# Kernel optimization log

Measured on AMD Instinct MI355X. Metric: run time of the kernel, lower is better.

Reference implementation:

```python
import jax, jax.numpy as jnp
import numpy as np

B, S, HID, NH = 2, 2048, 1024, 16
HD = HID // NH
SCALE = HD ** -0.5


def elu_plus_one(x):
    return jax.nn.elu(x) + 1.0


def setup_inputs() -> dict:
    key = jax.random.key(0)
    ks = jax.random.split(key, 8)
    w_scale = 0.02  # keep logits in a sane range
    return {
        "hidden_states": jax.random.normal(ks[0], (B, S, HID), jnp.float32),
        "wq": jax.random.normal(ks[1], (HID, HID), jnp.float32) * w_scale,
        "wk": jax.random.normal(ks[2], (HID, HID), jnp.float32) * w_scale,
        "wv": jax.random.normal(ks[3], (HID, HID), jnp.float32) * w_scale,
        "wo": jax.random.normal(ks[4], (HID, HID), jnp.float32) * w_scale,
        "beta": jax.random.normal(ks[5], (NH,), jnp.float32),
        "memory": jax.random.normal(ks[6], (NH, HD, HD), jnp.float32),
        "memory_norm": jax.random.uniform(ks[7], (NH, HD), jnp.float32),
    }


def reference(hidden_states, wq, wk, wv, wo, beta, memory, memory_norm):
    b, s, _ = hidden_states.shape
    # nn.Linear(bias=False): x @ W^T; weights stored [out, in]
    def proj(x, w):
        return jnp.einsum("bsh,oh->bso", x, w).reshape(b, s, NH, HD).transpose(0, 2, 1, 3)

    q = proj(hidden_states, wq)  # [B,H,S,D]
    k = proj(hidden_states, wk)
    v = proj(hidden_states, wv)

    # local causal softmax attention (materializes [B,H,S,S] as the original does)
    scores = jnp.einsum("bhsd,bhtd->bhst", q, k) * SCALE
    causal_mask = jnp.triu(jnp.full((s, s), -jnp.inf, dtype=scores.dtype), k=1)
    attn = jax.nn.softmax(scores + causal_mask, axis=-1)
    a_local = jnp.einsum("bhst,bhtd->bhsd", attn, v)

    # compressive memory retrieval: sigma(Q) @ M / (sigma(Q) @ z)
    sigma_q = elu_plus_one(q)
    a_mem_unnorm = jnp.einsum("bhsd,hde->bhse", sigma_q, memory)
    norm = jnp.clip(jnp.einsum("bhsd,hd->bhs", sigma_q, memory_norm), 1e-6, None)
    a_mem = a_mem_unnorm / norm[..., None]

    gate = jax.nn.sigmoid(beta).reshape(1, NH, 1, 1)
    combined = gate * a_mem + (1.0 - gate) * a_local  # [B,H,S,D]
    combined = combined.transpose(0, 2, 1, 3).reshape(b, s, HID)
    return jnp.einsum("bsh,oh->bso", combined, wo)
```

## Files before the change

kernel.cpp:

```cpp
#include <hip/hip_runtime.h>
#include <stdint.h>

#define LOG2E 1.4426950408889634f

typedef __attribute__((ext_vector_type(8))) __bf16 bf16x8;
typedef __attribute__((ext_vector_type(4))) __bf16 bf16x4;
typedef __attribute__((ext_vector_type(4))) float f32x4;

__device__ inline void gll16(const void* g, void* l) {
  __builtin_amdgcn_global_load_lds(
      (const __attribute__((address_space(1))) void*)g,
      (__attribute__((address_space(3))) void*)l, 16, 0, 0);
}

__global__ __launch_bounds__(256) void cvt_all(
    const float* __restrict__ hs, const float* __restrict__ wq,
    const float* __restrict__ wk, const float* __restrict__ wv,
    const float* __restrict__ wo,
    __bf16* __restrict__ hsb, __bf16* __restrict__ wqb, __bf16* __restrict__ wkb,
    __bf16* __restrict__ wvb, __bf16* __restrict__ wob) {
  int bid = blockIdx.x;
  const float* s; __bf16* d; int i;
  if (bid < 4096) { s = hs; d = hsb; i = bid * 256 + threadIdx.x; }
  else {
    int seg = (bid - 4096) >> 10;
    i = ((bid - 4096) & 1023) * 256 + threadIdx.x;
    s = seg == 0 ? wq : seg == 1 ? wk : seg == 2 ? wv : wo;
    d = seg == 0 ? wqb : seg == 1 ? wkb : seg == 2 ? wvb : wob;
  }
  float4 v = ((const float4*)s)[i];
  bf16x4 o;
  o[0] = (__bf16)v.x; o[1] = (__bf16)v.y; o[2] = (__bf16)v.z; o[3] = (__bf16)v.w;
  *(bf16x4*)&d[(size_t)i * 4] = o;
}

#define KSCALE 0.18033688011112042f
__global__ __launch_bounds__(256, 3) void qkv_gemm(
    const __bf16* __restrict__ hsb, const __bf16* __restrict__ wqb,
    const __bf16* __restrict__ wkb, const __bf16* __restrict__ wvb,
    __bf16* __restrict__ qbuf, __bf16* __restrict__ kbuf,
    __bf16* __restrict__ vtb) {
  constexpr int K = 1024;
  __shared__ __align__(16) __bf16 lta[128 * 32];
  __shared__ __align__(16) __bf16 ltb[128 * 32];
  const int bid = blockIdx.x;
  const int z = bid >> 8, r = bid & 255;
  const __bf16 *A, *Bt;
  int m0, n0;
  if (z < 2) {
    A = hsb; Bt = z ? wkb : wqb;
    m0 = (r & 31) * 128; n0 = (r >> 5) * 128;
  } else {
    A = wvb; Bt = hsb;
    m0 = (r & 7) * 128; n0 = (r >> 3) * 128;
  }
  const int tid = threadIdx.x;
  const int w = tid >> 6, l = tid & 63;
  const int lg = l >> 4, lr = l & 15;
  const int wm = (w >> 1) * 64, wn = (w & 1) * 64;
  f32x4 acc[4][4] = {};
  const int srow = w * 16 + (l >> 2);
  const int scol = (l & 3) * 8;
  const __bf16* ga = A + (size_t)(m0 + srow) * K + scol;
  const __bf16* gb = Bt + (size_t)(n0 + srow) * K + scol;
  __bf16* la = &lta[(size_t)w * 16 * 32];
  __bf16* lb = &ltb[(size_t)w * 16 * 32];
  for (int k0 = 0; k0 < K; k0 += 32) {
    __syncthreads();
    gll16(ga + k0, la);
    gll16(ga + 64 * K + k0, la + 64 * 32);
    gll16(gb + k0, lb);
    gll16(gb + 64 * K + k0, lb + 64 * 32);
    __syncthreads();
    bf16x8 af[4], bfr[4];
#pragma unroll
    for (int i = 0; i < 4; ++i) {
      af[i]  = *(const bf16x8*)&lta[(wm + i * 16 + lr) * 32 + lg * 8];
      bfr[i] = *(const bf16x8*)&ltb[(wn + i * 16 + lr) * 32 + lg * 8];
    }
#pragma unroll
    for (int i = 0; i < 4; ++i)
#pragma unroll
      for (int j = 0; j < 4; ++j)
        acc[i][j] = __builtin_amdgcn_mfma_f32_16x16x32_bf16(af[i], bfr[j], acc[i][j], 0, 0, 0);
  }
#pragma unroll
  for (int i = 0; i < 4; ++i)
#pragma unroll
    for (int j = 0; j < 4; ++j)
#pragma unroll
      for (int rr = 0; rr < 4; ++rr) {
        int gm = m0 + wm + i * 16 + lg * 4 + rr;
        int gn = n0 + wn + j * 16 + lr;
        float v = acc[i][j][rr];
        if (z < 2) {
          int bb = gm >> 11, s = gm & 2047, hh = gn >> 6, d = gn & 63;
          __bf16* dst = z ? kbuf : qbuf;
          if (z) v *= KSCALE;
          dst[(((size_t)bb * 16 + hh) * 2048 + s) * 64 + d] = (__bf16)v;
        } else {
          int bb = gn >> 11, s = gn & 2047, hh = gm >> 6, d = gm & 63;
          vtb[(((size_t)bb * 16 + hh) * 64 + d) * 2048 + s] = (__bf16)v;
        }
      }
}

__global__ __launch_bounds__(256, 2) void gemm_out(const __bf16* __restrict__ A,
                                                   const __bf16* __restrict__ Bt,
                                                   float* __restrict__ C,
                                                   int M, int N) {
  constexpr int K = 1024;
  __shared__ __align__(16) __bf16 lta[128 * 32];
  __shared__ __align__(16) __bf16 ltb[64 * 32];
  const int tid = threadIdx.x;
  const int w = tid >> 6, l = tid & 63;
  const int lg = l >> 4, lr = l & 15;
  const int m0 = blockIdx.x * 128, n0 = blockIdx.y * 64;
  const int wm = (w >> 1) * 64, wn = (w & 1) * 32;
  f32x4 acc[4][2] = {};
  const int srow = tid >> 2;
  const int scol = (tid & 3) * 8;
  const __bf16* ga = A + (size_t)(m0 + srow) * K + scol;
  const __bf16* gb = Bt + (size_t)(n0 + srow) * K + scol;
  __bf16* la = &lta[(size_t)w * 512];
  __bf16* lb = &ltb[(size_t)w * 512];
  for (int k0 = 0; k0 < K; k0 += 32) {
    __syncthreads();
    gll16(ga + k0, la);
    gll16(ga + (size_t)64 * K + k0, la + 64 * 32);
    gll16(gb + k0, lb);
    __syncthreads();
    bf16x8 af[4], bfr[2];
#pragma unroll
    for (int i = 0; i < 4; ++i)
      af[i]  = *(const bf16x8*)&lta[(wm + i * 16 + lr) * 32 + lg * 8];
#pragma unroll
    for (int j = 0; j < 2; ++j)
      bfr[j] = *(const bf16x8*)&ltb[(wn + j * 16 + lr) * 32 + lg * 8];
#pragma unroll
    for (int i = 0; i < 4; ++i)
#pragma unroll
      for (int j = 0; j < 2; ++j)
        acc[i][j] = __builtin_amdgcn_mfma_f32_16x16x32_bf16(af[i], bfr[j], acc[i][j], 0, 0, 0);
  }
#pragma unroll
  for (int i = 0; i < 4; ++i)
#pragma unroll
    for (int j = 0; j < 2; ++j)
#pragma unroll
      for (int rr = 0; rr < 4; ++rr) {
        int gm = m0 + wm + i * 16 + lg * 4 + rr;
        int gn = n0 + wn + j * 16 + lr;
        C[(size_t)gm * N + gn] = acc[i][j][rr];
      }
}

#define DEFER_THR 11.5f
#define SWZ(row, col) (((row) << 7) + ((col) ^ (((row) & 7) << 3)))
#define SWZK(row, col) (((row) << 6) + ((col) ^ (((row) & 7) << 3)))

__global__ __launch_bounds__(256, 2) void attn_kernel(
    const __bf16* __restrict__ qb,
    const __bf16* __restrict__ kb,
    const __bf16* __restrict__ vtb,
    const float* __restrict__ memory,
    const float* __restrict__ memnorm,
    const float* __restrict__ beta,
    __bf16* __restrict__ comb)
{
  __shared__ __align__(16) __bf16 kt[128 * 64];
  __shared__ __align__(16) __bf16 vt[64 * 128];
  __shared__ __align__(16) __bf16 pt[4][16 * 128];

  const int tid = threadIdx.x;
  const int w = tid >> 6, l = tid & 63;
  const int lg = l >> 4, lr = l & 15;
  const int tt = blockIdx.x >> 5;
  const int t = (tt < 8) ? (15 - tt) : (tt - 8);
  const int bh = blockIdx.x & 31;
  const int hh = bh & 15, b = bh >> 4;
  const int wq0 = t * 128 + w * 32;
  const int ntiles = t + 1;

  const int k_row = tid >> 3;
  const int k_col = ((tid & 7) ^ (k_row & 7)) * 8;
  const __bf16* ksrc = kb + ((size_t)bh * 2048 + k_row) * 64 + k_col;
  const int v_d = tid >> 4;
  const int v_col = ((tid & 15) ^ (v_d & 7)) * 8;
  const __bf16* vsrc = vtb + ((size_t)bh * 64 + v_d) * 2048 + v_col;
  __bf16* kdst = &kt[w * 512];
  __bf16* vdst = &vt[w * 512];

  bf16x8 qf[2][2];
#pragma unroll
  for (int mf = 0; mf < 2; ++mf)
#pragma unroll
    for (int kk = 0; kk < 2; ++kk)
      qf[mf][kk] = *(const bf16x8*)(qb + ((size_t)bh * 2048 + wq0 + mf * 16 + lr) * 64 + kk * 32 + lg * 8);

  float mrun[2] = {-1e30f, -1e30f}, lsum[2] = {0.f, 0.f};
  f32x4 apv[2][4] = {};

  for (int kv = 0; kv < ntiles; ++kv) {
    const int kv0 = kv * 128;
    __syncthreads();
#pragma unroll
    for (int i = 0; i < 4; ++i) {
      gll16(ksrc + (size_t)(kv0 + i * 32) * 64, kdst + i * 2048);
      gll16(vsrc + (size_t)i * 16 * 2048 + kv0, vdst + i * 2048);
    }
    __syncthreads();

    f32x4 sc[2][8] = {};
#pragma unroll
    for (int kk = 0; kk < 2; ++kk)
#pragma unroll
      for (int nf = 0; nf < 8; ++nf) {
        bf16x8 kf = *(const bf16x8*)&kt[SWZK(nf * 16 + lr, kk * 32 + lg * 8)];
#pragma unroll
        for (int mf = 0; mf < 2; ++mf)
          sc[mf][nf] = __builtin_amdgcn_mfma_f32_16x16x32_bf16(kf, qf[mf][kk], sc[mf][nf], 0, 0, 0);
      }

    if (kv == ntiles - 1) {
#pragma unroll
      for (int mf = 0; mf < 2; ++mf) {
        const int qrow = wq0 + mf * 16 + lr;
#pragma unroll
        for (int nf = 0; nf < 8; ++nf)
#pragma unroll
          for (int r = 0; r < 4; ++r)
            if (kv0 + nf * 16 + lg * 4 + r > qrow) sc[mf][nf][r] = -1e30f;
      }
    }

#pragma unroll
    for (int mf = 0; mf < 2; ++mf) {
      f32x4 m4 = sc[mf][0];
#pragma unroll
      for (int nf = 1; nf < 8; ++nf)
#pragma unroll
        for (int r = 0; r < 4; ++r) m4[r] = fmaxf(m4[r], sc[mf][nf][r]);
      float mx = fmaxf(fmaxf(m4[0], m4[1]), fmaxf(m4[2], m4[3]));
      mx = fmaxf(mx, __shfl_xor(mx, 16, 64));
      mx = fmaxf(mx, __shfl_xor(mx, 32, 64));
      if (!__all(mx - mrun[mf] <= DEFER_THR)) {
        float mold = mrun[mf];
        float mn = fmaxf(mold, mx);
        mrun[mf] = mn;
        float scl = __builtin_amdgcn_exp2f(mold - mn);
        lsum[mf] *= scl;
        float sclq[4];
#pragma unroll
        for (int r = 0; r < 4; ++r) sclq[r] = __shfl(scl, (lg << 2) | r, 16);
#pragma unroll
        for (int nf = 0; nf < 4; ++nf)
#pragma unroll
          for (int r = 0; r < 4; ++r) apv[mf][nf][r] *= sclq[r];
      }
    }

    bf16x8 pa0[4];
    {
      float rs = 0.f;
#pragma unroll
      for (int nf = 0; nf < 8; ++nf) {
        bf16x4 pk;
#pragma unroll
        for (int r = 0; r < 4; ++r) {
          float pv = __builtin_amdgcn_exp2f(sc[0][nf][r] - mrun[0]);
          rs += pv;
          pk[r] = (__bf16)pv;
        }
        *(bf16x4*)&pt[w][SWZ(lr, nf * 16 + lg * 4)] = pk;
      }
      rs += __shfl_xor(rs, 16, 64);
      rs += __shfl_xor(rs, 32, 64);
      lsum[0] += rs;
#pragma unroll
      for (int kk = 0; kk < 4; ++kk)
        pa0[kk] = *(const bf16x8*)&pt[w][SWZ(lr, kk * 32 + lg * 8)];
    }
    {
      float rs = 0.f;
#pragma unroll
      for (int nf = 0; nf < 8; ++nf) {
        bf16x4 pk;
#pragma unroll
        for (int r = 0; r < 4; ++r) {
          float pv = __builtin_amdgcn_exp2f(sc[1][nf][r] - mrun[1]);
          rs += pv;
          pk[r] = (__bf16)pv;
        }
        *(bf16x4*)&pt[w][SWZ(lr, nf * 16 + lg * 4)] = pk;
      }
      rs += __shfl_xor(rs, 16, 64);
      rs += __shfl_xor(rs, 32, 64);
      lsum[1] += rs;
    }

#pragma unroll
    for (int kk = 0; kk < 4; ++kk) {
      bf16x8 pa1 = *(const bf16x8*)&pt[w][SWZ(lr, kk * 32 + lg * 8)];
#pragma unroll
      for (int nf = 0; nf < 4; ++nf) {
        bf16x8 vf = *(const bf16x8*)&vt[SWZ(nf * 16 + lr, kk * 32 + lg * 8)];
        apv[0][nf] = __builtin_amdgcn_mfma_f32_16x16x32_bf16(pa0[kk], vf, apv[0][nf], 0, 0, 0);
        apv[1][nf] = __builtin_amdgcn_mfma_f32_16x16x32_bf16(pa1, vf, apv[1][nf], 0, 0, 0);
      }
    }
  }

  __syncthreads();
  __bf16* mt = kt;
  for (int i = tid; i < 64 * 64; i += 256) {
    int d = i >> 6, e = i & 63;
    mt[e * 72 + d] = (__bf16)memory[((size_t)hh * 64 + d) * 64 + e];
  }
  for (int i = tid; i < 16 * 64; i += 256) {
    int e = 64 + (i >> 6), d = i & 63;
    mt[e * 72 + d] = (__bf16)memnorm[hh * 64 + d];
  }
  __syncthreads();

  bf16x8 sf[2][2];
#pragma unroll
  for (int mf = 0; mf < 2; ++mf)
#pragma unroll
    for (int kk = 0; kk < 2; ++kk) {
      bf16x8 q = qf[mf][kk], s;
#pragma unroll
      for (int j = 0; j < 8; ++j) {
        float x = (float)q[j];
        float sg = x > 0.f ? x + 1.f : __builtin_amdgcn_exp2f(x * LOG2E);
        s[j] = (__bf16)sg;
      }
      sf[mf][kk] = s;
    }

  f32x4 am[2][5] = {};
#pragma unroll
  for (int kk = 0; kk < 2; ++kk)
#pragma unroll
    for (int nf = 0; nf < 5; ++nf) {
      bf16x8 bb = *(const bf16x8*)&mt[(nf * 16 + lr) * 72 + kk * 32 + lg * 8];
#pragma unroll
      for (int mf = 0; mf < 2; ++mf)
        am[mf][nf] = __builtin_amdgcn_mfma_f32_16x16x32_bf16(sf[mf][kk], bb, am[mf][nf], 0, 0, 0);
    }

  const float gate = 1.f / (1.f + __builtin_amdgcn_exp2f(-beta[hh] * LOG2E));
  const float og = 1.f - gate;
#pragma unroll
  for (int mf = 0; mf < 2; ++mf) {
    float lsq[4];
#pragma unroll
    for (int r = 0; r < 4; ++r) lsq[r] = __shfl(lsum[mf], (lg << 2) | r, 16);
#pragma unroll
    for (int r = 0; r < 4; ++r) {
      int row = wq0 + mf * 16 + lg * 4 + r;
      float linv = __builtin_amdgcn_rcpf(lsq[r]);
      float nrm = fmaxf(am[mf][4][r], 1e-6f);
      float ninv = __builtin_amdgcn_rcpf(nrm);
      size_t base = ((size_t)b * 2048 + row) * 1024 + hh * 64;
#pragma unroll
      for (int nf = 0; nf < 4; ++nf)
        comb[base + nf * 16 + lr] =
            (__bf16)(gate * am[mf][nf][r] * ninv + og * apv[mf][nf][r] * linv);
    }
  }
}

extern "C" void kernel_launch(void* const* d_in, const int* in_sizes, int n_in,
                              void* d_out, int out_size, void* d_ws, size_t ws_size,
                              hipStream_t stream) {
  const float* hs      = (const float*)d_in[0];
  const float* wq      = (const float*)d_in[1];
  const float* wk      = (const float*)d_in[2];
  const float* wv      = (const float*)d_in[3];
  const float* wo      = (const float*)d_in[4];
  const float* beta    = (const float*)d_in[5];
  const float* memory  = (const float*)d_in[6];
  const float* memnorm = (const float*)d_in[7];
  float* out = (float*)d_out;

  char* ws = (char*)d_ws;
  __bf16* hsb  = (__bf16*)(ws);
  __bf16* wqb  = (__bf16*)(ws + ((size_t)8  << 20));
  __bf16* wkb  = (__bf16*)(ws + ((size_t)10 << 20));
  __bf16* wvb  = (__bf16*)(ws + ((size_t)12 << 20));
  __bf16* wob  = (__bf16*)(ws + ((size_t)14 << 20));
  __bf16* qbuf = (__bf16*)(ws + ((size_t)16 << 20));
  __bf16* kbuf = (__bf16*)(ws + ((size_t)24 << 20));
  __bf16* vtb  = (__bf16*)(ws + ((size_t)32 << 20));
  __bf16* comb = (__bf16*)(ws + ((size_t)40 << 20));

  cvt_all<<<8192, 256, 0, stream>>>(hs, wq, wk, wv, wo, hsb, wqb, wkb, wvb, wob);

  qkv_gemm<<<768, 256, 0, stream>>>(hsb, wqb, wkb, wvb, qbuf, kbuf, vtb);

  attn_kernel<<<512, 256, 0, stream>>>(qbuf, kbuf, vtb, memory, memnorm, beta, comb);

  gemm_out<<<dim3(32, 16), 256, 0, stream>>>(comb, wob, out, 4096, 1024);
}
```

Before: 110.4 us.

## Double-buffer K/V tiles in LDS to overlap global loads with compute

Doubles the K and V LDS buffers and prefetches the next KV tile with global_load_lds while the current tile is computed, cutting one barrier per iteration. The loads of tile kv+1 are meant to hide behind the QK and PV MFMA work. It also splits the row-sum accumulation into four independent partial sums to shorten the dependency chain. LDS use per block rises from about 48KB to 80KB, which may limit the two-blocks-per-CU occupancy the launch bounds request.

Measured after the change: 115.2 us. +4.4%, slower.

```diff
diff --git a/kernel.cpp b/kernel.cpp
--- a/kernel.cpp
+++ b/kernel.cpp
@@ -168,8 +168,8 @@
     const float* __restrict__ beta,
     __bf16* __restrict__ comb)
 {
-  __shared__ __align__(16) __bf16 kt[128 * 64];
-  __shared__ __align__(16) __bf16 vt[64 * 128];
+  __shared__ __align__(16) __bf16 kt[2][128 * 64];
+  __shared__ __align__(16) __bf16 vt[2][64 * 128];
   __shared__ __align__(16) __bf16 pt[4][16 * 128];
 
   const int tid = threadIdx.x;
@@ -188,8 +188,6 @@
   const int v_d = tid >> 4;
   const int v_col = ((tid & 15) ^ (v_d & 7)) * 8;
   const __bf16* vsrc = vtb + ((size_t)bh * 64 + v_d) * 2048 + v_col;
-  __bf16* kdst = &kt[w * 512];
-  __bf16* vdst = &vt[w * 512];
 
   bf16x8 qf[2][2];
 #pragma unroll
@@ -198,25 +196,38 @@
     for (int kk = 0; kk < 2; ++kk)
       qf[mf][kk] = *(const bf16x8*)(qb + ((size_t)bh * 2048 + wq0 + mf * 16 + lr) * 64 + kk * 32 + lg * 8);
 
+#pragma unroll
+  for (int i = 0; i < 4; ++i) {
+    gll16(ksrc + (size_t)(i * 32) * 64, &kt[0][w * 512] + i * 2048);
+    gll16(vsrc + (size_t)i * 16 * 2048, &vt[0][w * 512] + i * 2048);
+  }
+
   float mrun[2] = {-1e30f, -1e30f}, lsum[2] = {0.f, 0.f};
   f32x4 apv[2][4] = {};
+  int cur = 0;
 
   for (int kv = 0; kv < ntiles; ++kv) {
+    asm volatile("s_waitcnt vmcnt(0)" ::: "memory");
+    __syncthreads();
+    if (kv + 1 < ntiles) {
+      const int nxt = cur ^ 1;
+      const int kvn = (kv + 1) * 128;
+#pragma unroll
+      for (int i = 0; i < 4; ++i) {
+        gll16(ksrc + (size_t)(kvn + i * 32) * 64, &kt[nxt][w * 512] + i * 2048);
+        gll16(vsrc + (size_t)i * 16 * 2048 + kvn, &vt[nxt][w * 512] + i * 2048);
+      }
+    }
     const int kv0 = kv * 128;
-    __syncthreads();
-#pragma unroll
-    for (int i = 0; i < 4; ++i) {
-      gll16(ksrc + (size_t)(kv0 + i * 32) * 64, kdst + i * 2048);
-      gll16(vsrc + (size_t)i * 16 * 2048 + kv0, vdst + i * 2048);
-    }
-    __syncthreads();
+    const __bf16* ktc = &kt[cur][0];
+    const __bf16* vtc = &vt[cur][0];
 
     f32x4 sc[2][8] = {};
 #pragma unroll
     for (int kk = 0; kk < 2; ++kk)
 #pragma unroll
       for (int nf = 0; nf < 8; ++nf) {
-        bf16x8 kf = *(const bf16x8*)&kt[SWZK(nf * 16 + lr, kk * 32 + lg * 8)];
+        bf16x8 kf = *(const bf16x8*)&ktc[SWZK(nf * 16 + lr, kk * 32 + lg * 8)];
 #pragma unroll
         for (int mf = 0; mf < 2; ++mf)
           sc[mf][nf] = __builtin_amdgcn_mfma_f32_16x16x32_bf16(kf, qf[mf][kk], sc[mf][nf], 0, 0, 0);
@@ -262,18 +273,19 @@
 
     bf16x8 pa0[4];
     {
-      float rs = 0.f;
+      f32x4 rs4 = {0.f, 0.f, 0.f, 0.f};
 #pragma unroll
       for (int nf = 0; nf < 8; ++nf) {
         bf16x4 pk;
 #pragma unroll
         for (int r = 0; r < 4; ++r) {
           float pv = __builtin_amdgcn_exp2f(sc[0][nf][r] - mrun[0]);
-          rs += pv;
+          rs4[r] += pv;
           pk[r] = (__bf16)pv;
         }
         *(bf16x4*)&pt[w][SWZ(lr, nf * 16 + lg * 4)] = pk;
       }
+      float rs = (rs4[0] + rs4[1]) + (rs4[2] + rs4[3]);
       rs += __shfl_xor(rs, 16, 64);
       rs += __shfl_xor(rs, 32, 64);
       lsum[0] += rs;
@@ -282,18 +294,19 @@
         pa0[kk] = *(const bf16x8*)&pt[w][SWZ(lr, kk * 32 + lg * 8)];
     }
     {
-      float rs = 0.f;
+      f32x4 rs4 = {0.f, 0.f, 0.f, 0.f};
 #pragma unroll
       for (int nf = 0; nf < 8; ++nf) {
         bf16x4 pk;
 #pragma unroll
         for (int r = 0; r < 4; ++r) {
           float pv = __builtin_amdgcn_exp2f(sc[1][nf][r] - mrun[1]);
-          rs += pv;
+          rs4[r] += pv;
           pk[r] = (__bf16)pv;
         }
         *(bf16x4*)&pt[w][SWZ(lr, nf * 16 + lg * 4)] = pk;
       }
+      float rs = (rs4[0] + rs4[1]) + (rs4[2] + rs4[3]);
       rs += __shfl_xor(rs, 16, 64);
       rs += __shfl_xor(rs, 32, 64);
       lsum[1] += rs;
@@ -304,15 +317,16 @@
       bf16x8 pa1 = *(const bf16x8*)&pt[w][SWZ(lr, kk * 32 + lg * 8)];
 #pragma unroll
       for (int nf = 0; nf < 4; ++nf) {
-        bf16x8 vf = *(const bf16x8*)&vt[SWZ(nf * 16 + lr, kk * 32 + lg * 8)];
+        bf16x8 vf = *(const bf16x8*)&vtc[SWZ(nf * 16 + lr, kk * 32 + lg * 8)];
         apv[0][nf] = __builtin_amdgcn_mfma_f32_16x16x32_bf16(pa0[kk], vf, apv[0][nf], 0, 0, 0);
         apv[1][nf] = __builtin_amdgcn_mfma_f32_16x16x32_bf16(pa1, vf, apv[1][nf], 0, 0, 0);
       }
     }
+    cur ^= 1;
   }
 
   __syncthreads();
-  __bf16* mt = kt;
+  __bf16* mt = &kt[0][0];
   for (int i = tid; i < 64 * 64; i += 256) {
     int d = i >> 6, e = i & 63;
     mt[e * 72 + d] = (__bf16)memory[((size_t)hh * 64 + d) * 64 + e];
```
